# Optimization experiments

Hardware: AMD Instinct MI355X
Metric: run time of the kernel (lower is better)

## Reference

```python
import jax, jax.numpy as jnp
import numpy as np

N_NODES = 50000
N_EDGES = 800000
NEG_SLOPE = 0.2


def _gat_layer(x, src, dst, W, a_src, a_dst, b, heads, out_ch, num_nodes):
    # Linear projection per head: [N, H, C]
    h = (x @ W).reshape(num_nodes, heads, out_ch)
    # Per-node attention logits [N, H]
    al_src = jnp.sum(h * a_src, axis=-1)
    al_dst = jnp.sum(h * a_dst, axis=-1)
    # Per-edge scores, LeakyReLU as in PyG GATConv: alpha_j (src) + alpha_i (dst)
    e = jax.nn.leaky_relu(al_src[src] + al_dst[dst], NEG_SLOPE)  # [E, H]
    # Segment softmax over incoming edges of each destination node
    m = jax.ops.segment_max(e, dst, num_segments=num_nodes)       # [N, H]
    e = jnp.exp(e - m[dst])
    denom = jax.ops.segment_sum(e, dst, num_segments=num_nodes)   # [N, H]
    alpha = e / (denom[dst] + 1e-16)                              # [E, H]
    # Attention-weighted aggregation: scatter-add messages to destinations
    out = jax.ops.segment_sum(h[src] * alpha[:, :, None], dst, num_segments=num_nodes)
    return out.reshape(num_nodes, heads * out_ch) + b


def _forward(x, edge_index, W1, a_src1, a_dst1, b1, W2, a_src2, a_dst2, b2, W3, a_src3, a_dst3, b3):
    n = x.shape[0]
    loops = jnp.arange(n, dtype=edge_index.dtype)
    src = jnp.concatenate([edge_index[0], loops])
    dst = jnp.concatenate([edge_index[1], loops])
    h = _gat_layer(x, src, dst, W1, a_src1, a_dst1, b1, 4, 64, n)
    h = jax.nn.elu(h)
    h = _gat_layer(h, src, dst, W2, a_src2, a_dst2, b2, 2, 64, n)
    h = jax.nn.elu(h)
    h = _gat_layer(h, src, dst, W3, a_src3, a_dst3, b3, 1, 16, n)
    return jax.nn.log_softmax(h, axis=1)


def setup_inputs() -> dict:
    key = jax.random.key(0)
    ks = jax.random.split(key, 12)
    s = lambda fan: 1.0 / np.sqrt(fan)
    return {
        "x": jax.random.normal(ks[0], (N_NODES, 128), dtype=jnp.float32),
        "edge_index": jax.random.randint(ks[1], (2, N_EDGES), 0, N_NODES, dtype=jnp.int64),
        "W1": jax.random.normal(ks[2], (128, 256), dtype=jnp.float32) * s(128),
        "a_src1": jax.random.normal(ks[3], (4, 64), dtype=jnp.float32) * s(64),
        "a_dst1": jax.random.normal(ks[4], (4, 64), dtype=jnp.float32) * s(64),
        "b1": jnp.zeros((256,), dtype=jnp.float32),
        "W2": jax.random.normal(ks[5], (256, 128), dtype=jnp.float32) * s(256),
        "a_src2": jax.random.normal(ks[6], (2, 64), dtype=jnp.float32) * s(64),
        "a_dst2": jax.random.normal(ks[7], (2, 64), dtype=jnp.float32) * s(64),
        "b2": jnp.zeros((128,), dtype=jnp.float32),
        "W3": jax.random.normal(ks[8], (128, 16), dtype=jnp.float32) * s(128),
        "a_src3": jax.random.normal(ks[9], (1, 16), dtype=jnp.float32) * s(16),
        "a_dst3": jax.random.normal(ks[10], (1, 16), dtype=jnp.float32) * s(16),
        "b3": jnp.zeros((16,), dtype=jnp.float32),
    }


def reference(x, edge_index, W1, a_src1, a_dst1, b1, W2, a_src2, a_dst2, b2, W3, a_src3, a_dst3, b3):
    return _forward(x, edge_index, W1, a_src1, a_dst1, b1, W2, a_src2, a_dst2, b2, W3, a_src3, a_dst3, b3)
```

## Files before the change

### kernel.cpp

```cpp
#include <hip/hip_runtime.h>
#include <math.h>


#define NEG_SLOPE 0.2f

typedef __attribute__((ext_vector_type(8))) short short8;
typedef __attribute__((ext_vector_type(4))) float f32x4;

__device__ inline unsigned short f2bf(float f) {
    union { float f; unsigned u; } c{f};
    unsigned r = (c.u + 0x7FFFu + ((c.u >> 16) & 1u)) >> 16;
    return (unsigned short)r;
}
__device__ inline float bflo(unsigned u) {
    union { unsigned u; float f; } c{u << 16};
    return c.f;
}
__device__ inline float bfhi(unsigned u) {
    union { unsigned u; float f; } c{u & 0xFFFF0000u};
    return c.f;
}
__device__ inline float bf2f(unsigned short v) {
    union { unsigned u; float f; } c{(unsigned)v << 16};
    return c.f;
}

__global__ __launch_bounds__(256) void mega_prep_kernel(
        const unsigned int* __restrict__ w,
        const float* __restrict__ x,
        const float* __restrict__ W1,
        const float* __restrict__ W2,
        const float* __restrict__ W3,
        int* __restrict__ src32,
        int* __restrict__ dst32,
        int* __restrict__ counts,
        unsigned short* __restrict__ xbf,
        unsigned short* __restrict__ WT1,
        unsigned short* __restrict__ WT2,
        unsigned short* __restrict__ WT3,
        int E, int NN, int xn4) {
    const int TOT = E + NN;
    int i = blockIdx.x * 256 + threadIdx.x;

    __shared__ int nz;
    bool edge_block = (blockIdx.x * 256 < TOT);
    int is64 = 0;
    if (edge_block) {
        if (threadIdx.x == 0) nz = 0;
        __syncthreads();
        if (w[2 * threadIdx.x + 1] != 0) atomicAdd(&nz, 1);
        __syncthreads();
        is64 = (nz == 0) ? 1 : 0;
    }

    if (i < TOT) {
        int s, d;
        if (i < E) {
            if (is64) {
                s = (int)w[2 * (size_t)i];
                d = (int)w[2 * ((size_t)E + i)];
            } else {
                s = (int)w[i];
                d = (int)w[E + i];
            }
        } else {
            s = d = i - E;
        }
        src32[i] = s;
        dst32[i] = d;
        atomicAdd(&counts[d], 1);
        return;
    }
    int j = i - TOT;
    if (j < xn4) {
        float4 v = reinterpret_cast<const float4*>(x)[j];
        ushort4 o;
        o.x = f2bf(v.x); o.y = f2bf(v.y); o.z = f2bf(v.z); o.w = f2bf(v.w);
        reinterpret_cast<ushort4*>(xbf)[j] = o;
        return;
    }
    j -= xn4;
    if (j < 128 * 256) {
        int k = j / 256, n = j % 256;
        WT1[(size_t)n * 128 + k] = f2bf(W1[j]);
        return;
    }
    j -= 128 * 256;
    if (j < 256 * 128) {
        int k = j / 128, n = j % 128;
        WT2[(size_t)n * 256 + k] = f2bf(W2[j]);
        return;
    }
    j -= 256 * 128;
    if (j < 128 * 16) {
        int k = j / 16, n = j % 16;
        WT3[(size_t)n * 128 + k] = f2bf(W3[j]);
    }
}

__global__ __launch_bounds__(256) void scan_partial(const int* __restrict__ counts,
                                                    int* __restrict__ bsum, int n) {
    int i = blockIdx.x * 256 + threadIdx.x;
    int v = (i < n) ? counts[i] : 0;
    for (int d = 1; d < 64; d <<= 1) v += __shfl_xor(v, d);
    __shared__ int ws[4];
    if ((threadIdx.x & 63) == 0) ws[threadIdx.x >> 6] = v;
    __syncthreads();
    if (threadIdx.x == 0) bsum[blockIdx.x] = ws[0] + ws[1] + ws[2] + ws[3];
}

__global__ __launch_bounds__(256) void scan_write(const int* __restrict__ counts,
                                                  const int* __restrict__ bsum,
                                                  int* __restrict__ offsets,
                                                  int* __restrict__ cursor,
                                                  int n, int nb) {
    int t = threadIdx.x;
    int bv = (t < blockIdx.x && t < nb) ? bsum[t] : 0;
    for (int d = 1; d < 64; d <<= 1) bv += __shfl_xor(bv, d);
    __shared__ int wb[4];
    if ((t & 63) == 0) wb[t >> 6] = bv;
    __syncthreads();
    int base0 = wb[0] + wb[1] + wb[2] + wb[3];

    int i = blockIdx.x * 256 + t;
    int v = (i < n) ? counts[i] : 0;
    int lane = t & 63, w = t >> 6;
    int sc = v;
    for (int d = 1; d < 64; d <<= 1) {
        int u = __shfl_up(sc, d);
        if (lane >= d) sc += u;
    }
    __shared__ int wsum[4];
    if (lane == 63) wsum[w] = sc;
    __syncthreads();
    int base = base0;
    for (int j = 0; j < w; ++j) base += wsum[j];
    int excl = base + sc - v;
    if (i < n) {
        offsets[i] = excl;
        cursor[i] = excl;
        if (i == n - 1) offsets[n] = excl + v;
    }
}

__global__ __launch_bounds__(256) void scatter_kernel(const int* __restrict__ src32,
                                                      const int* __restrict__ dst32,
                                                      int* __restrict__ cursor,
                                                      int* __restrict__ csr_src,
                                                      int total) {
    int i = blockIdx.x * 256 + threadIdx.x;
    if (i >= total) return;
    int d = dst32[i];
    int pos = atomicAdd(&cursor[d], 1);
    csr_src[pos] = src32[i];
}

template <int K, int N, int C>
__global__ __launch_bounds__(256) void gemm_mfma_al(const unsigned short* __restrict__ Xbf,
                                                    const unsigned short* __restrict__ WT,
                                                    unsigned short* __restrict__ Hbf,
                                                    const float* __restrict__ a_src,
                                                    const float* __restrict__ a_dst,
                                                    float* __restrict__ alS,
                                                    float* __restrict__ alD,
                                                    int M) {
    constexpr int KK = K / 32;
    constexpr int HH = N / C;
    constexpr int SEG = C / 16;
    int wave = threadIdx.x >> 6;
    int lane = threadIdx.x & 63;
    int row0 = blockIdx.x * 64 + wave * 16;
    int rowA = row0 + (lane & 15);
    int kb = (lane >> 4) * 8;
    short8 a[KK];
    if (rowA < M) {
#pragma unroll
        for (int kk = 0; kk < KK; ++kk)
            a[kk] = *reinterpret_cast<const short8*>(&Xbf[(size_t)rowA * K + kk * 32 + kb]);
    } else {
#pragma unroll
        for (int kk = 0; kk < KK; ++kk)
            a[kk] = short8{0, 0, 0, 0, 0, 0, 0, 0};
    }
    int col = lane & 15;
    int rbase = row0 + ((lane >> 4) << 2);
    bool full = (rbase + 3) < M;
    float ps[4] = {0.f, 0.f, 0.f, 0.f};
    float pd[4] = {0.f, 0.f, 0.f, 0.f};
#pragma unroll
    for (int nc = 0; nc < N / 16; ++nc) {
        f32x4 acc = {0.f, 0.f, 0.f, 0.f};
#pragma unroll
        for (int kk = 0; kk < KK; ++kk) {
            short8 b = *reinterpret_cast<const short8*>(&WT[(size_t)(nc * 16 + col) * K + kk * 32 + kb]);
            acc = __builtin_amdgcn_mfma_f32_16x16x32_bf16(a[kk], b, acc, 0, 0, 0);
        }
        int j = nc * 16 + col;
        float asj = a_src[j], adj = a_dst[j];
#pragma unroll
        for (int r = 0; r < 4; ++r) {
            unsigned short hb = f2bf(acc[r]);
            if (full || (rbase + r < M))
                Hbf[(size_t)(rbase + r) * N + j] = hb;
            float hv = bf2f(hb);
            ps[r] = fmaf(hv, asj, ps[r]);
            pd[r] = fmaf(hv, adj, pd[r]);
        }
        if ((nc % SEG) == SEG - 1) {
            int head = nc / SEG;
#pragma unroll
            for (int r = 0; r < 4; ++r) {
                for (int d = 1; d < 16; d <<= 1) {
                    ps[r] += __shfl_xor(ps[r], d);
                    pd[r] += __shfl_xor(pd[r], d);
                }
            }
            if ((lane & 15) == 0) {
#pragma unroll
                for (int r = 0; r < 4; ++r) {
                    if (rbase + r < M) {
                        alS[(size_t)(rbase + r) * HH + head] = ps[r];
                        alD[(size_t)(rbase + r) * HH + head] = pd[r];
                    }
                }
            }
#pragma unroll
            for (int r = 0; r < 4; ++r) { ps[r] = 0.f; pd[r] = 0.f; }
        }
    }
}

template <int H, int C, int ACT>
__global__ __launch_bounds__(256) void aggf_kernel(const unsigned short* __restrict__ hbf,
                                                   const float* __restrict__ alS,
                                                   const float* __restrict__ alD,
                                                   const int* __restrict__ offsets,
                                                   const int* __restrict__ csr_src,
                                                   const float* __restrict__ bias,
                                                   unsigned short* __restrict__ outbf,
                                                   float* __restrict__ outf,
                                                   int NN) {
    constexpr int HC = H * C;
    constexpr int HC8 = HC / 8;
    constexpr int NPB = 256 / HC8;
    int g = threadIdx.x / HC8;
    int l8 = threadIdx.x % HC8;
    int hd = (l8 * 8) / C;
    int node = blockIdx.x * NPB + g;
    if (node >= NN) return;
    int beg = offsets[node];
    int end = offsets[node + 1];
    float ad = alD[(size_t)node * H + hd];
    const uint4* __restrict__ h4 = reinterpret_cast<const uint4*>(hbf);

    float acc[8];
#pragma unroll
    for (int k = 0; k < 8; ++k) acc[k] = 0.f;
    float s = 0.f;

#define EDGE_P(sn, pv)                                      \
    {                                                       \
        float e_ = alS[(size_t)(sn) * H + hd] + ad;         \
        e_ = (e_ > 0.f) ? e_ : NEG_SLOPE * e_;              \
        pv = __expf(e_);                                    \
    }
#define ACC8(vv, pp)                                        \
        acc[0] = fmaf(pp, bflo(vv.x), acc[0]);              \
        acc[1] = fmaf(pp, bfhi(vv.x), acc[1]);              \
        acc[2] = fmaf(pp, bflo(vv.y), acc[2]);              \
        acc[3] = fmaf(pp, bfhi(vv.y), acc[3]);              \
        acc[4] = fmaf(pp, bflo(vv.z), acc[4]);              \
        acc[5] = fmaf(pp, bfhi(vv.z), acc[5]);              \
        acc[6] = fmaf(pp, bflo(vv.w), acc[6]);              \
        acc[7] = fmaf(pp, bfhi(vv.w), acc[7]);

    int i = beg;
    for (; i + 4 <= end; i += 4) {
        int sn0 = csr_src[i + 0];
        int sn1 = csr_src[i + 1];
        int sn2 = csr_src[i + 2];
        int sn3 = csr_src[i + 3];
        uint4 v0 = h4[(size_t)sn0 * HC8 + l8];
        uint4 v1 = h4[(size_t)sn1 * HC8 + l8];
        uint4 v2 = h4[(size_t)sn2 * HC8 + l8];
        uint4 v3 = h4[(size_t)sn3 * HC8 + l8];
        float p0, p1, p2, p3;
        EDGE_P(sn0, p0)
        EDGE_P(sn1, p1)
        EDGE_P(sn2, p2)
        EDGE_P(sn3, p3)
        s += (p0 + p1) + (p2 + p3);
        ACC8(v0, p0)
        ACC8(v1, p1)
        ACC8(v2, p2)
        ACC8(v3, p3)
    }
    for (; i < end; ++i) {
        int sn = csr_src[i];
        uint4 v = h4[(size_t)sn * HC8 + l8];
        float p;
        EDGE_P(sn, p)
        s += p;
        ACC8(v, p)
    }
#undef ACC8
#undef EDGE_P

    float rs = 1.f / (s + 1e-16f);
    float val[8];
#pragma unroll
    for (int k = 0; k < 8; ++k)
        val[k] = acc[k] * rs + bias[l8 * 8 + k];
    if constexpr (ACT == 1) {
#pragma unroll
        for (int k = 0; k < 8; ++k)
            val[k] = (val[k] > 0.f) ? val[k] : expm1f(val[k]);
        uint4 o;
        o.x = (unsigned)f2bf(val[0]) | ((unsigned)f2bf(val[1]) << 16);
        o.y = (unsigned)f2bf(val[2]) | ((unsigned)f2bf(val[3]) << 16);
        o.z = (unsigned)f2bf(val[4]) | ((unsigned)f2bf(val[5]) << 16);
        o.w = (unsigned)f2bf(val[6]) | ((unsigned)f2bf(val[7]) << 16);
        reinterpret_cast<uint4*>(outbf)[(size_t)node * HC8 + l8] = o;
    }
    if constexpr (ACT == 2) {
        float mx = val[0];
#pragma unroll
        for (int k = 1; k < 8; ++k) mx = fmaxf(mx, val[k]);
        mx = fmaxf(mx, __shfl_xor(mx, 1, 2));
        float sm = 0.f;
#pragma unroll
        for (int k = 0; k < 8; ++k) sm += __expf(val[k] - mx);
        sm += __shfl_xor(sm, 1, 2);
        float lg = mx + logf(sm);
#pragma unroll
        for (int k = 0; k < 8; ++k) val[k] -= lg;
        float4* o4 = reinterpret_cast<float4*>(outf) + (size_t)node * (HC / 4) + l8 * 2;
        o4[0] = make_float4(val[0], val[1], val[2], val[3]);
        o4[1] = make_float4(val[4], val[5], val[6], val[7]);
    }
}

extern "C" void kernel_launch(void* const* d_in, const int* in_sizes, int n_in,
                              void* d_out, int out_size, void* d_ws, size_t ws_size,
                              hipStream_t stream) {
    const float* x = (const float*)d_in[0];
    const unsigned int* ei = (const unsigned int*)d_in[1];
    const float* W1 = (const float*)d_in[2];
    const float* as1 = (const float*)d_in[3];
    const float* ad1 = (const float*)d_in[4];
    const float* b1 = (const float*)d_in[5];
    const float* W2 = (const float*)d_in[6];
    const float* as2 = (const float*)d_in[7];
    const float* ad2 = (const float*)d_in[8];
    const float* b2 = (const float*)d_in[9];
    const float* W3 = (const float*)d_in[10];
    const float* as3 = (const float*)d_in[11];
    const float* ad3 = (const float*)d_in[12];
    const float* b3 = (const float*)d_in[13];
    float* out = (float*)d_out;

    const int NN = in_sizes[0] / 128;
    const int E = in_sizes[1] / 2;
    const int TOT = E + NN;

    char* base = (char*)d_ws;
    size_t off = 0;
    auto take = [&](size_t bytes) -> void* {
        void* p = base + off;
        off += (bytes + 255) & ~(size_t)255;
        return p;
    };
    int* offsets = (int*)take((size_t)(NN + 1) * 4);
    int* csr_src = (int*)take((size_t)TOT * 4);
    float* alS = (float*)take((size_t)NN * 4 * 4);
    float* alD = (float*)take((size_t)NN * 4 * 4);
    unsigned short* xbf = (unsigned short*)take((size_t)NN * 128 * 2);
    unsigned short* hbf = (unsigned short*)take((size_t)NN * 256 * 2);
    unsigned short* aggbf = (unsigned short*)take((size_t)NN * 256 * 2);
    unsigned short* WT1 = (unsigned short*)take(256 * 128 * 2);
    unsigned short* WT2 = (unsigned short*)take(128 * 256 * 2);
    unsigned short* WT3 = (unsigned short*)take(16 * 128 * 2);
    int* bsum = (int*)take(1024 * 4);
    int* src32 = (int*)take((size_t)TOT * 4);
    int* dst32 = (int*)take((size_t)TOT * 4);
    int* counts = (int*)take((size_t)NN * 4);
    int* cursor = (int*)take((size_t)NN * 4);
    (void)ws_size;

    int egrid = (TOT + 255) / 256;
    int sgrid = (NN + 255) / 256;
    int ggrid = (NN + 63) / 64;
    int grid_agg1 = NN / 8;
    int grid_agg2 = NN / 16;
    int grid_agg3 = (NN + 127) / 128;
    int xn4 = NN * 128 / 4;
    int mega_total = TOT + xn4 + 128 * 256 + 256 * 128 + 128 * 16;
    int mgrid = (mega_total + 255) / 256;

    hipMemsetAsync(counts, 0, (size_t)NN * 4, stream);
    mega_prep_kernel<<<mgrid, 256, 0, stream>>>(ei, x, W1, W2, W3,
                                                src32, dst32, counts,
                                                xbf, WT1, WT2, WT3, E, NN, xn4);
    scan_partial<<<sgrid, 256, 0, stream>>>(counts, bsum, NN);
    scan_write<<<sgrid, 256, 0, stream>>>(counts, bsum, offsets, cursor, NN, sgrid);
    scatter_kernel<<<egrid, 256, 0, stream>>>(src32, dst32, cursor, csr_src, TOT);

    gemm_mfma_al<128, 256, 64><<<ggrid, 256, 0, stream>>>(xbf, WT1, hbf, as1, ad1, alS, alD, NN);
    aggf_kernel<4, 64, 1><<<grid_agg1, 256, 0, stream>>>(hbf, alS, alD, offsets, csr_src, b1, aggbf, nullptr, NN);

    gemm_mfma_al<256, 128, 64><<<ggrid, 256, 0, stream>>>(aggbf, WT2, hbf, as2, ad2, alS, alD, NN);
    aggf_kernel<2, 64, 1><<<grid_agg2, 256, 0, stream>>>(hbf, alS, alD, offsets, csr_src, b2, aggbf, nullptr, NN);

    gemm_mfma_al<128, 16, 16><<<ggrid, 256, 0, stream>>>(aggbf, WT3, hbf, as3, ad3, alS, alD, NN);
    aggf_kernel<1, 16, 2><<<grid_agg3, 256, 0, stream>>>(hbf, alS, alD, offsets, csr_src, b3, nullptr, out, NN);
}
```

Before: 380.2 us.

## Stage weight tiles in LDS and compute two row groups per wave in GEMM

```diff
diff --git a/kernel.cpp b/kernel.cpp
--- a/kernel.cpp
+++ b/kernel.cpp
@@ -167,66 +167,103 @@
     constexpr int KK = K / 32;
     constexpr int HH = N / C;
     constexpr int SEG = C / 16;
+    constexpr int CHN = (N >= 32) ? 32 : 16;
+    constexpr int KP = K + 8;
+    __shared__ unsigned short blds[CHN * KP];
+
     int wave = threadIdx.x >> 6;
     int lane = threadIdx.x & 63;
-    int row0 = blockIdx.x * 64 + wave * 16;
-    int rowA = row0 + (lane & 15);
+    int row0 = blockIdx.x * 128 + wave * 32;
     int kb = (lane >> 4) * 8;
-    short8 a[KK];
-    if (rowA < M) {
-#pragma unroll
-        for (int kk = 0; kk < KK; ++kk)
-            a[kk] = *reinterpret_cast<const short8*>(&Xbf[(size_t)rowA * K + kk * 32 + kb]);
-    } else {
-#pragma unroll
-        for (int kk = 0; kk < KK; ++kk)
-            a[kk] = short8{0, 0, 0, 0, 0, 0, 0, 0};
-    }
     int col = lane & 15;
-    int rbase = row0 + ((lane >> 4) << 2);
-    bool full = (rbase + 3) < M;
-    float ps[4] = {0.f, 0.f, 0.f, 0.f};
-    float pd[4] = {0.f, 0.f, 0.f, 0.f};
-#pragma unroll
-    for (int nc = 0; nc < N / 16; ++nc) {
-        f32x4 acc = {0.f, 0.f, 0.f, 0.f};
-#pragma unroll
-        for (int kk = 0; kk < KK; ++kk) {
-            short8 b = *reinterpret_cast<const short8*>(&WT[(size_t)(nc * 16 + col) * K + kk * 32 + kb]);
-            acc = __builtin_amdgcn_mfma_f32_16x16x32_bf16(a[kk], b, acc, 0, 0, 0);
+
+    short8 a[2][KK];
+#pragma unroll
+    for (int rg = 0; rg < 2; ++rg) {
+        int rowA = row0 + rg * 16 + col;
+        if (rowA < M) {
+#pragma unroll
+            for (int kk = 0; kk < KK; ++kk)
+                a[rg][kk] = *reinterpret_cast<const short8*>(&Xbf[(size_t)rowA * K + kk * 32 + kb]);
+        } else {
+#pragma unroll
+            for (int kk = 0; kk < KK; ++kk)
+                a[rg][kk] = short8{0, 0, 0, 0, 0, 0, 0, 0};
         }
-        int j = nc * 16 + col;
-        float asj = a_src[j], adj = a_dst[j];
-#pragma unroll
-        for (int r = 0; r < 4; ++r) {
-            unsigned short hb = f2bf(acc[r]);
-            if (full || (rbase + r < M))
-                Hbf[(size_t)(rbase + r) * N + j] = hb;
-            float hv = bf2f(hb);
-            ps[r] = fmaf(hv, asj, ps[r]);
-            pd[r] = fmaf(hv, adj, pd[r]);
+    }
+
+    float ps[2][4] = {{0.f, 0.f, 0.f, 0.f}, {0.f, 0.f, 0.f, 0.f}};
+    float pd[2][4] = {{0.f, 0.f, 0.f, 0.f}, {0.f, 0.f, 0.f, 0.f}};
+
+    for (int ch = 0; ch < N / CHN; ++ch) {
+        constexpr int LD = CHN * K / 8;
+        for (int t = threadIdx.x; t < LD; t += 256) {
+            int c = t / (K / 8);
+            int k8 = t % (K / 8);
+            short8 v = *reinterpret_cast<const short8*>(&WT[(size_t)(ch * CHN + c) * K + k8 * 8]);
+            *reinterpret_cast<short8*>(&blds[c * KP + k8 * 8]) = v;
         }
-        if ((nc % SEG) == SEG - 1) {
-            int head = nc / SEG;
-#pragma unroll
-            for (int r = 0; r < 4; ++r) {
-                for (int d = 1; d < 16; d <<= 1) {
-                    ps[r] += __shfl_xor(ps[r], d);
-                    pd[r] += __shfl_xor(pd[r], d);
+        __syncthreads();
+#pragma unroll
+        for (int ncc = 0; ncc < CHN / 16; ++ncc) {
+            int nc = ch * (CHN / 16) + ncc;
+            f32x4 acc0 = {0.f, 0.f, 0.f, 0.f};
+            f32x4 acc1 = {0.f, 0.f, 0.f, 0.f};
+#pragma unroll
+            for (int kk = 0; kk < KK; ++kk) {
+                short8 b = *reinterpret_cast<const short8*>(&blds[(ncc * 16 + col) * KP + kk * 32 + kb]);
+                acc0 = __builtin_amdgcn_mfma_f32_16x16x32_bf16(a[0][kk], b, acc0, 0, 0, 0);
+                acc1 = __builtin_amdgcn_mfma_f32_16x16x32_bf16(a[1][kk], b, acc1, 0, 0, 0);
+            }
+            int j = nc * 16 + col;
+            float asj = a_src[j], adj = a_dst[j];
+#pragma unroll
+            for (int rg = 0; rg < 2; ++rg) {
+                int rbase = row0 + rg * 16 + ((lane >> 4) << 2);
+                const f32x4& acc = rg ? acc1 : acc0;
+                bool full = (rbase + 3) < M;
+#pragma unroll
+                for (int r = 0; r < 4; ++r) {
+                    unsigned short hb = f2bf(acc[r]);
+                    if (full || (rbase + r < M))
+                        Hbf[(size_t)(rbase + r) * N + j] = hb;
+                    float hv = bf2f(hb);
+                    ps[rg][r] = fmaf(hv, asj, ps[rg][r]);
+                    pd[rg][r] = fmaf(hv, adj, pd[rg][r]);
                 }
             }
-            if ((lane & 15) == 0) {
-#pragma unroll
-                for (int r = 0; r < 4; ++r) {
-                    if (rbase + r < M) {
-                        alS[(size_t)(rbase + r) * HH + head] = ps[r];
-                        alD[(size_t)(rbase + r) * HH + head] = pd[r];
+            if ((nc % SEG) == SEG - 1) {
+                int head = nc / SEG;
+#pragma unroll
+                for (int rg = 0; rg < 2; ++rg) {
+#pragma unroll
+                    for (int r = 0; r < 4; ++r) {
+                        for (int d = 1; d < 16; d <<= 1) {
+                            ps[rg][r] += __shfl_xor(ps[rg][r], d);
+                            pd[rg][r] += __shfl_xor(pd[rg][r], d);
+                        }
                     }
                 }
+                if (col == 0) {
+#pragma unroll
+                    for (int rg = 0; rg < 2; ++rg) {
+                        int rbase = row0 + rg * 16 + ((lane >> 4) << 2);
+#pragma unroll
+                        for (int r = 0; r < 4; ++r) {
+                            if (rbase + r < M) {
+                                alS[(size_t)(rbase + r) * HH + head] = ps[rg][r];
+                                alD[(size_t)(rbase + r) * HH + head] = pd[rg][r];
+                            }
+                        }
+                    }
+                }
+#pragma unroll
+                for (int rg = 0; rg < 2; ++rg)
+#pragma unroll
+                    for (int r = 0; r < 4; ++r) { ps[rg][r] = 0.f; pd[rg][r] = 0.f; }
             }
-#pragma unroll
-            for (int r = 0; r < 4; ++r) { ps[r] = 0.f; pd[r] = 0.f; }
         }
+        __syncthreads();
     }
 }
 
@@ -389,7 +426,7 @@
 
     int egrid = (TOT + 255) / 256;
     int sgrid = (NN + 255) / 256;
-    int ggrid = (NN + 63) / 64;
+    int ggrid = (NN + 127) / 128;
     int grid_agg1 = NN / 8;
     int grid_agg2 = NN / 16;
     int grid_agg3 = (NN + 127) / 128;
```

Result: faster. 339.6 us (-10.7%).
